# Kernel optimization log

Hardware: AMD Instinct MI355X
Metric: run time of the kernel (lower is better)

Reference implementation:

```python
import jax, jax.numpy as jnp
import numpy as np

N = 50000      # number of nodes
E = 800000     # number of edges (avg degree 16)
DIN = 128
DOUT = 128
EPS = 1e-06


def setup_inputs() -> dict:
    key = jax.random.key(0)
    ks = jax.random.split(key, 10)
    scale = 1.0 / np.sqrt(DIN)
    return {
        "mean": jax.random.normal(ks[0], (N, DIN), dtype=jnp.float32),
        "var": jax.random.uniform(ks[1], (N, DIN), dtype=jnp.float32),
        "W_mean": jax.random.normal(ks[2], (DIN, DOUT), dtype=jnp.float32) * scale,
        "b_mean": jax.random.normal(ks[3], (DOUT,), dtype=jnp.float32) * scale,
        "W_var": jax.random.normal(ks[4], (DIN, DOUT), dtype=jnp.float32) * scale,
        "b_var": jax.random.normal(ks[5], (DOUT,), dtype=jnp.float32) * scale,
        "adj0_w": jax.random.uniform(ks[6], (E,), dtype=jnp.float32),
        "adj1_w": jax.random.uniform(ks[7], (E,), dtype=jnp.float32),
        "edge_src": jax.random.randint(ks[8], (E,), 0, N, dtype=jnp.int32),
        "edge_dst": jax.random.randint(ks[9], (E,), 0, N, dtype=jnp.int32),
    }


def reference(mean, var, W_mean, b_mean, W_var, b_var, adj0_w, adj1_w, edge_src, edge_dst):
    # Dense projections (dropout is identity in eval mode)
    m = jax.nn.elu(mean @ W_mean + b_mean)            # [N, DOUT]
    v = jax.nn.relu(var @ W_var + b_var) + EPS        # [N, DOUT]
    # Elementwise attention gate
    att = jnp.exp(-v)
    m = m * att
    v = v * att * att
    # SpMM aggregation: out[dst] += w * x[src]  (COO edge list)
    n = mean.shape[0]
    out_m = jax.ops.segment_sum(adj0_w[:, None] * m[edge_src], edge_dst, num_segments=n)
    out_v = jax.ops.segment_sum(adj1_w[:, None] * v[edge_src], edge_dst, num_segments=n)
    return out_m, out_v
```

## Files before the change

kernel.cpp:

```cpp
#include <hip/hip_runtime.h>
#include <hip/hip_bf16.h>
#include <math.h>

#define N_NODES 50000
#define DIN     128
#define DOUT    128
#define EPS_    1e-6f
#define N_WAVES 3125
#define NBKT    196
#define EPB     4096
#define SLOT_CAP 5120

typedef __attribute__((ext_vector_type(8))) short  bf16x8;
typedef __attribute__((ext_vector_type(4))) float  f32x4;
typedef unsigned short ushort_t;

__device__ __forceinline__ ushort_t f2bf(float f) {
    unsigned u = __float_as_uint(f);
    return (ushort_t)((u + 0x7fffu + ((u >> 16) & 1u)) >> 16);
}
__device__ __forceinline__ float bflo(unsigned u) { return __uint_as_float(u << 16); }
__device__ __forceinline__ float bfhi(unsigned u) { return __uint_as_float(u & 0xffff0000u); }

__global__ __launch_bounds__(256) void prep_w_kernel(
    const float* __restrict__ Wm, const float* __restrict__ Wv,
    ushort_t* __restrict__ fm, ushort_t* __restrict__ fv,
    int* __restrict__ gcur)
{
    const int gid = blockIdx.x * 256 + threadIdx.x;
    if (gid < NBKT) gcur[gid] = 0;
    const int k = gid >> 7, n = gid & 127;
    const int ct = n >> 4, kk = k >> 5, quad = (k >> 3) & 3, j = k & 7;
    const int idx = ((ct * 4 + kk) * 64 + quad * 16 + (n & 15)) * 8 + j;
    fm[idx] = f2bf(Wm[gid]);
    fv[idx] = f2bf(Wv[gid]);
}

__global__ __launch_bounds__(256) void proj_mfma_kernel(
    const float* __restrict__ mean, const float* __restrict__ var,
    const float* __restrict__ bm,   const float* __restrict__ bv,
    const ushort_t* __restrict__ wfm, const ushort_t* __restrict__ wfv,
    ushort_t* __restrict__ mv)
{
    const int wave = blockIdx.x * 4 + (threadIdx.x >> 6);
    if (wave >= N_WAVES) return;
    const int lane = threadIdx.x & 63;
    const int row0 = wave * 16;
    const int kq   = lane >> 4;
    const int arow = row0 + (lane & 15);

    f32x4 accm[8], accv[8];
#pragma unroll
    for (int ct = 0; ct < 8; ++ct) {
        accm[ct] = (f32x4){0.f, 0.f, 0.f, 0.f};
        accv[ct] = (f32x4){0.f, 0.f, 0.f, 0.f};
    }

    const float* mrow = mean + (size_t)arow * DIN;
    const float* vrow = var  + (size_t)arow * DIN;

#pragma unroll
    for (int kk = 0; kk < 4; ++kk) {
        const int kb = kk * 32 + kq * 8;
        const float4 am0 = *(const float4*)(mrow + kb);
        const float4 am1 = *(const float4*)(mrow + kb + 4);
        const float4 av0 = *(const float4*)(vrow + kb);
        const float4 av1 = *(const float4*)(vrow + kb + 4);
        bf16x8 a_m, a_v;
        a_m[0]=f2bf(am0.x); a_m[1]=f2bf(am0.y); a_m[2]=f2bf(am0.z); a_m[3]=f2bf(am0.w);
        a_m[4]=f2bf(am1.x); a_m[5]=f2bf(am1.y); a_m[6]=f2bf(am1.z); a_m[7]=f2bf(am1.w);
        a_v[0]=f2bf(av0.x); a_v[1]=f2bf(av0.y); a_v[2]=f2bf(av0.z); a_v[3]=f2bf(av0.w);
        a_v[4]=f2bf(av1.x); a_v[5]=f2bf(av1.y); a_v[6]=f2bf(av1.z); a_v[7]=f2bf(av1.w);

#pragma unroll
        for (int ct = 0; ct < 8; ++ct) {
            const bf16x8 b_m = *(const bf16x8*)(wfm + ((size_t)(ct * 4 + kk) * 64 + lane) * 8);
            const bf16x8 b_v = *(const bf16x8*)(wfv + ((size_t)(ct * 4 + kk) * 64 + lane) * 8);
            accm[ct] = __builtin_amdgcn_mfma_f32_16x16x32_bf16(a_m, b_m, accm[ct], 0, 0, 0);
            accv[ct] = __builtin_amdgcn_mfma_f32_16x16x32_bf16(a_v, b_v, accv[ct], 0, 0, 0);
        }
    }

#pragma unroll
    for (int ct = 0; ct < 8; ++ct) {
        const int col = ct * 16 + (lane & 15);
        const float bmc = bm[col];
        const float bvc = bv[col];
        const int pbase = (col >> 1) * 4 + (col & 1);
#pragma unroll
        for (int r = 0; r < 4; ++r) {
            const int row = row0 + kq * 4 + r;
            float m = accm[ct][r] + bmc;
            m = (m > 0.0f) ? m : (expf(m) - 1.0f);
            float v = accv[ct][r] + bvc;
            v = ((v > 0.0f) ? v : 0.0f) + EPS_;
            const float att = expf(-v);
            ushort_t* rowp = mv + (size_t)row * 256;
            rowp[pbase]     = f2bf(m * att);
            rowp[pbase + 2] = f2bf(v * att * att);
        }
    }
}

__global__ __launch_bounds__(256) void bucketA_kernel(
    const int* __restrict__ src, const int* __restrict__ dst,
    const float* __restrict__ w0, const float* __restrict__ w1,
    int* __restrict__ gcur, uint2* __restrict__ slots, int E)
{
    __shared__ uint2 s_rec[EPB];
    __shared__ int   s_gpos[EPB];
    __shared__ int   s_hist[256];
    __shared__ int   s_scn[256];
    __shared__ int   s_cur[256];
    __shared__ int   s_base[256];

    const int t  = threadIdx.x;
    const int e0 = blockIdx.x * EPB;
    const int n  = min(EPB, E - e0);

    s_hist[t] = 0;
    __syncthreads();

    int   myb[16];
    uint2 myr[16];
#pragma unroll
    for (int j = 0; j < 16; ++j) {
        const int e = e0 + t + j * 256;
        if (e < E) {
            const int d = dst[e];
            const int b = d >> 8;
            myb[j] = b;
            myr[j].x = (unsigned)src[e] | ((unsigned)(d & 255) << 16);
            myr[j].y = (unsigned)f2bf(w0[e]) | ((unsigned)f2bf(w1[e]) << 16);
            atomicAdd(&s_hist[b], 1);
        } else myb[j] = -1;
    }
    __syncthreads();

    if (t < NBKT) {
        const int c = s_hist[t];
        s_base[t] = t * SLOT_CAP + (c ? atomicAdd(&gcur[t], c) : 0);
    }
    const int x = s_hist[t];
    s_scn[t] = x;
    __syncthreads();
    for (int off = 1; off < 256; off <<= 1) {
        const int v = (t >= off) ? s_scn[t - off] : 0;
        __syncthreads();
        s_scn[t] += v;
        __syncthreads();
    }
    const int excl = s_scn[t] - x;
    __syncthreads();
    s_scn[t] = excl;
    s_cur[t] = 0;
    __syncthreads();

#pragma unroll
    for (int j = 0; j < 16; ++j) {
        if (myb[j] >= 0) {
            const int r = atomicAdd(&s_cur[myb[j]], 1);
            const int p = s_scn[myb[j]] + r;
            s_rec[p]  = myr[j];
            s_gpos[p] = s_base[myb[j]] + r;
        }
    }
    __syncthreads();

    for (int i = t; i < n; i += 256)
        slots[s_gpos[i]] = s_rec[i];
}

__global__ __launch_bounds__(256) void bucketB_kernel(
    const int* __restrict__ gcur,
    const uint2* __restrict__ slots, uint2* __restrict__ final_e,
    int* __restrict__ node_start)
{
    __shared__ int s_hist[256];
    __shared__ int s_scn[256];
    __shared__ int s_cur[256];
    __shared__ int s_red[256];

    const int b = blockIdx.x;
    const int t = threadIdx.x;

    s_red[t] = (t < b) ? gcur[t] : 0;
    s_hist[t] = 0;
    __syncthreads();
    for (int off = 128; off > 0; off >>= 1) {
        if (t < off) s_red[t] += s_red[t + off];
        __syncthreads();
    }
    const int base = s_red[0];
    const int cnt  = gcur[b];
    const uint2* slot = slots + (size_t)b * SLOT_CAP;

    uint2 myr[20];
    int   myf[20];
    int   k = 0;
    for (int i = t; i < cnt; i += 256) {
        const uint2 r = slot[i];
        const int f = (r.x >> 16) & 255;
        myr[k] = r; myf[k] = f; ++k;
        atomicAdd(&s_hist[f], 1);
    }
    __syncthreads();

    const int x = s_hist[t];
    s_scn[t] = x;
    __syncthreads();
    for (int off = 1; off < 256; off <<= 1) {
        const int v = (t >= off) ? s_scn[t - off] : 0;
        __syncthreads();
        s_scn[t] += v;
        __syncthreads();
    }
    const int excl = s_scn[t] - x;
    __syncthreads();

    const int gidx = b * 256 + t;
    if (gidx <= N_NODES) node_start[gidx] = base + excl;

    s_cur[t] = excl;
    __syncthreads();

#pragma unroll
    for (int j = 0; j < 20; ++j) {
        if (j < k) {
            const int p = atomicAdd(&s_cur[myf[j]], 1);
            final_e[base + p] = myr[j];
        }
    }
}

#define PAIR_FMA(RW, G) do {                                                 \
    const float a0 = bflo(RW), a1 = bfhi(RW);                                \
    am0 = fmaf(a0, bflo((G).x), am0); am1 = fmaf(a0, bfhi((G).x), am1);      \
    av0 = fmaf(a1, bflo((G).y), av0); av1 = fmaf(a1, bfhi((G).y), av1);      \
    am2 = fmaf(a0, bflo((G).z), am2); am3 = fmaf(a0, bfhi((G).z), am3);      \
    av2 = fmaf(a1, bflo((G).w), av2); av3 = fmaf(a1, bfhi((G).w), av3);      \
} while (0)

__global__ __launch_bounds__(256) void agg_kernel(
    const ushort_t* __restrict__ mv,
    const uint2* __restrict__ edges, const int* __restrict__ node_start,
    float* __restrict__ out_m, float* __restrict__ out_v)
{
    const int node = blockIdx.x * 4 + (threadIdx.x >> 6);
    const int lane = threadIdx.x & 63;
    const int half = lane >> 5;
    const int l    = lane & 31;
    if (node >= N_NODES) return;

    const int j0 = node_start[node];
    const int j1 = node_start[node + 1];

    float am0=0.f, am1=0.f, am2=0.f, am3=0.f;
    float av0=0.f, av1=0.f, av2=0.f, av3=0.f;

    int j = j0;

    if ((j & 1) && j < j1) {
        const uint2 r = edges[j];
        const unsigned rw = half ? 0u : r.y;
        const uint4 g = *(const uint4*)(mv + (size_t)(r.x & 0xffffu) * 256 + l * 8);
        PAIR_FMA(rw, g);
        ++j;
    }

    for (; j + 8 <= j1; j += 8) {
        const uint4 e0 = *(const uint4*)(edges + j + 0);
        const uint4 e1 = *(const uint4*)(edges + j + 2);
        const uint4 e2 = *(const uint4*)(edges + j + 4);
        const uint4 e3 = *(const uint4*)(edges + j + 6);
        const unsigned s0 = half ? e0.z : e0.x, w0 = half ? e0.w : e0.y;
        const unsigned s1 = half ? e1.z : e1.x, w1 = half ? e1.w : e1.y;
        const unsigned s2 = half ? e2.z : e2.x, w2 = half ? e2.w : e2.y;
        const unsigned s3 = half ? e3.z : e3.x, w3 = half ? e3.w : e3.y;
        const uint4 g0 = *(const uint4*)(mv + (size_t)(s0 & 0xffffu) * 256 + l * 8);
        const uint4 g1 = *(const uint4*)(mv + (size_t)(s1 & 0xffffu) * 256 + l * 8);
        const uint4 g2 = *(const uint4*)(mv + (size_t)(s2 & 0xffffu) * 256 + l * 8);
        const uint4 g3 = *(const uint4*)(mv + (size_t)(s3 & 0xffffu) * 256 + l * 8);
        PAIR_FMA(w0, g0);
        PAIR_FMA(w1, g1);
        PAIR_FMA(w2, g2);
        PAIR_FMA(w3, g3);
    }

    for (; j + 2 <= j1; j += 2) {
        const uint4 e = *(const uint4*)(edges + j);
        const unsigned s = half ? e.z : e.x, w = half ? e.w : e.y;
        const uint4 g = *(const uint4*)(mv + (size_t)(s & 0xffffu) * 256 + l * 8);
        PAIR_FMA(w, g);
    }

    if (j < j1) {
        const uint2 r = edges[j];
        const unsigned rw = half ? 0u : r.y;
        const uint4 g = *(const uint4*)(mv + (size_t)(r.x & 0xffffu) * 256 + l * 8);
        PAIR_FMA(rw, g);
    }

    am0 += __shfl_xor(am0, 32); am1 += __shfl_xor(am1, 32);
    am2 += __shfl_xor(am2, 32); am3 += __shfl_xor(am3, 32);
    av0 += __shfl_xor(av0, 32); av1 += __shfl_xor(av1, 32);
    av2 += __shfl_xor(av2, 32); av3 += __shfl_xor(av3, 32);

    if (half == 0) {
        *(float4*)(out_m + (size_t)node * DOUT + l * 4) = make_float4(am0, am1, am2, am3);
        *(float4*)(out_v + (size_t)node * DOUT + l * 4) = make_float4(av0, av1, av2, av3);
    }
}

extern "C" void kernel_launch(void* const* d_in, const int* in_sizes, int n_in,
                              void* d_out, int out_size, void* d_ws, size_t ws_size,
                              hipStream_t stream) {
    const float* mean = (const float*)d_in[0];
    const float* var  = (const float*)d_in[1];
    const float* Wm   = (const float*)d_in[2];
    const float* bm   = (const float*)d_in[3];
    const float* Wv   = (const float*)d_in[4];
    const float* bv   = (const float*)d_in[5];
    const float* a0   = (const float*)d_in[6];
    const float* a1   = (const float*)d_in[7];
    const int*   es   = (const int*)d_in[8];
    const int*   ed   = (const int*)d_in[9];
    const int    E    = in_sizes[6];

    char* ws = (char*)d_ws;
    ushort_t* mv        = (ushort_t*)ws;
    uint2* slots        = (uint2*)(ws + 25600000);
    uint2* final_e      = (uint2*)(ws + 33628160);
    int*   node_start   = (int*)  (ws + 40028160);
    int*   gcur         = (int*)  (ws + 40228176);
    ushort_t* wfm       = (ushort_t*)(ws + 40228976);
    ushort_t* wfv       = wfm + 16384;

    float* out_m = (float*)d_out;
    float* out_v = out_m + (size_t)N_NODES * DOUT;

    prep_w_kernel<<<64, 256, 0, stream>>>(Wm, Wv, wfm, wfv, gcur);

    proj_mfma_kernel<<<(N_WAVES + 3) / 4, 256, 0, stream>>>(
        mean, var, bm, bv, wfm, wfv, mv);

    bucketA_kernel<<<(E + EPB - 1) / EPB, 256, 0, stream>>>(
        es, ed, a0, a1, gcur, slots, E);
    bucketB_kernel<<<NBKT, 256, 0, stream>>>(
        gcur, slots, final_e, node_start);

    agg_kernel<<<(N_NODES + 3) / 4, 256, 0, stream>>>(
        mv, final_e, node_start, out_m, out_v);
}
```

Baseline: 232.7 us.

## Fuse projection and edge bucketing into one launch; stream bucketB from global

Merges the MFMA projection kernel and the first edge-bucketing pass into a single launch, with the first nA blocks doing bucketing and the rest doing projection. The two independent phases can then overlap on the GPU and one launch is saved. The cost is that the projection blocks now carry the bucketing kernel's large shared-memory allocation, which may lower occupancy. bucketB also stops caching records in registers and re-reads each slot from global memory in a second pass, cutting register use at the price of an extra read.

```diff
diff --git a/kernel.cpp b/kernel.cpp
--- a/kernel.cpp
+++ b/kernel.cpp
@@ -10,6 +10,7 @@
 #define NBKT    196
 #define EPB     4096
 #define SLOT_CAP 5120
+#define NB_PROJ 782
 
 typedef __attribute__((ext_vector_type(8))) short  bf16x8;
 typedef __attribute__((ext_vector_type(4))) float  f32x4;
@@ -36,13 +37,82 @@
     fv[idx] = f2bf(Wv[gid]);
 }
 
-__global__ __launch_bounds__(256) void proj_mfma_kernel(
+__global__ __launch_bounds__(256) void fused_projA_kernel(
     const float* __restrict__ mean, const float* __restrict__ var,
     const float* __restrict__ bm,   const float* __restrict__ bv,
     const ushort_t* __restrict__ wfm, const ushort_t* __restrict__ wfv,
-    ushort_t* __restrict__ mv)
+    ushort_t* __restrict__ mv,
+    const int* __restrict__ src, const int* __restrict__ dst,
+    const float* __restrict__ w0, const float* __restrict__ w1,
+    int* __restrict__ gcur, uint2* __restrict__ slots, int E, int nA)
 {
-    const int wave = blockIdx.x * 4 + (threadIdx.x >> 6);
+    if ((int)blockIdx.x < nA) {
+        __shared__ uint2 s_rec[EPB];
+        __shared__ int   s_gpos[EPB];
+        __shared__ int   s_hist[256];
+        __shared__ int   s_scn[256];
+        __shared__ int   s_cur[256];
+        __shared__ int   s_base[256];
+
+        const int t  = threadIdx.x;
+        const int e0 = blockIdx.x * EPB;
+        const int n  = min(EPB, E - e0);
+
+        s_hist[t] = 0;
+        __syncthreads();
+
+        int   myb[16];
+        uint2 myr[16];
+#pragma unroll
+        for (int j = 0; j < 16; ++j) {
+            const int e = e0 + t + j * 256;
+            if (e < E) {
+                const int d = dst[e];
+                const int b = d >> 8;
+                myb[j] = b;
+                myr[j].x = (unsigned)src[e] | ((unsigned)(d & 255) << 16);
+                myr[j].y = (unsigned)f2bf(w0[e]) | ((unsigned)f2bf(w1[e]) << 16);
+                atomicAdd(&s_hist[b], 1);
+            } else myb[j] = -1;
+        }
+        __syncthreads();
+
+        if (t < NBKT) {
+            const int c = s_hist[t];
+            s_base[t] = t * SLOT_CAP + (c ? atomicAdd(&gcur[t], c) : 0);
+        }
+        const int x = s_hist[t];
+        s_scn[t] = x;
+        __syncthreads();
+        for (int off = 1; off < 256; off <<= 1) {
+            const int v = (t >= off) ? s_scn[t - off] : 0;
+            __syncthreads();
+            s_scn[t] += v;
+            __syncthreads();
+        }
+        const int excl = s_scn[t] - x;
+        __syncthreads();
+        s_scn[t] = excl;
+        s_cur[t] = 0;
+        __syncthreads();
+
+#pragma unroll
+        for (int j = 0; j < 16; ++j) {
+            if (myb[j] >= 0) {
+                const int r = atomicAdd(&s_cur[myb[j]], 1);
+                const int p = s_scn[myb[j]] + r;
+                s_rec[p]  = myr[j];
+                s_gpos[p] = s_base[myb[j]] + r;
+            }
+        }
+        __syncthreads();
+
+        for (int i = t; i < n; i += 256)
+            slots[s_gpos[i]] = s_rec[i];
+        return;
+    }
+
+    const int wave = ((int)blockIdx.x - nA) * 4 + (threadIdx.x >> 6);
     if (wave >= N_WAVES) return;
     const int lane = threadIdx.x & 63;
     const int row0 = wave * 16;
@@ -102,75 +172,6 @@
     }
 }
 
-__global__ __launch_bounds__(256) void bucketA_kernel(
-    const int* __restrict__ src, const int* __restrict__ dst,
-    const float* __restrict__ w0, const float* __restrict__ w1,
-    int* __restrict__ gcur, uint2* __restrict__ slots, int E)
-{
-    __shared__ uint2 s_rec[EPB];
-    __shared__ int   s_gpos[EPB];
-    __shared__ int   s_hist[256];
-    __shared__ int   s_scn[256];
-    __shared__ int   s_cur[256];
-    __shared__ int   s_base[256];
-
-    const int t  = threadIdx.x;
-    const int e0 = blockIdx.x * EPB;
-    const int n  = min(EPB, E - e0);
-
-    s_hist[t] = 0;
-    __syncthreads();
-
-    int   myb[16];
-    uint2 myr[16];
-#pragma unroll
-    for (int j = 0; j < 16; ++j) {
-        const int e = e0 + t + j * 256;
-        if (e < E) {
-            const int d = dst[e];
-            const int b = d >> 8;
-            myb[j] = b;
-            myr[j].x = (unsigned)src[e] | ((unsigned)(d & 255) << 16);
-            myr[j].y = (unsigned)f2bf(w0[e]) | ((unsigned)f2bf(w1[e]) << 16);
-            atomicAdd(&s_hist[b], 1);
-        } else myb[j] = -1;
-    }
-    __syncthreads();
-
-    if (t < NBKT) {
-        const int c = s_hist[t];
-        s_base[t] = t * SLOT_CAP + (c ? atomicAdd(&gcur[t], c) : 0);
-    }
-    const int x = s_hist[t];
-    s_scn[t] = x;
-    __syncthreads();
-    for (int off = 1; off < 256; off <<= 1) {
-        const int v = (t >= off) ? s_scn[t - off] : 0;
-        __syncthreads();
-        s_scn[t] += v;
-        __syncthreads();
-    }
-    const int excl = s_scn[t] - x;
-    __syncthreads();
-    s_scn[t] = excl;
-    s_cur[t] = 0;
-    __syncthreads();
-
-#pragma unroll
-    for (int j = 0; j < 16; ++j) {
-        if (myb[j] >= 0) {
-            const int r = atomicAdd(&s_cur[myb[j]], 1);
-            const int p = s_scn[myb[j]] + r;
-            s_rec[p]  = myr[j];
-            s_gpos[p] = s_base[myb[j]] + r;
-        }
-    }
-    __syncthreads();
-
-    for (int i = t; i < n; i += 256)
-        slots[s_gpos[i]] = s_rec[i];
-}
-
 __global__ __launch_bounds__(256) void bucketB_kernel(
     const int* __restrict__ gcur,
     const uint2* __restrict__ slots, uint2* __restrict__ final_e,
@@ -184,7 +185,7 @@
     const int b = blockIdx.x;
     const int t = threadIdx.x;
 
-    s_red[t] = (t < b) ? gcur[t] : 0;
+    s_red[t]  = (t < b) ? gcur[t] : 0;
     s_hist[t] = 0;
     __syncthreads();
     for (int off = 128; off > 0; off >>= 1) {
@@ -195,41 +196,33 @@
     const int cnt  = gcur[b];
     const uint2* slot = slots + (size_t)b * SLOT_CAP;
 
-    uint2 myr[20];
-    int   myf[20];
-    int   k = 0;
+    for (int i = t; i < cnt; i += 256)
+        atomicAdd(&s_hist[(slot[i].x >> 16) & 255], 1);
+    __syncthreads();
+
+    const int x = s_hist[t];
+    s_scn[t] = x;
+    __syncthreads();
+    for (int off = 1; off < 256; off <<= 1) {
+        const int v = (t >= off) ? s_scn[t - off] : 0;
+        __syncthreads();
+        s_scn[t] += v;
+        __syncthreads();
+    }
+    const int excl = s_scn[t] - x;
+    __syncthreads();
+
+    const int gidx = b * 256 + t;
+    if (gidx <= N_NODES) node_start[gidx] = base + excl;
+
+    s_cur[t] = excl;
+    __syncthreads();
+
     for (int i = t; i < cnt; i += 256) {
         const uint2 r = slot[i];
         const int f = (r.x >> 16) & 255;
-        myr[k] = r; myf[k] = f; ++k;
-        atomicAdd(&s_hist[f], 1);
-    }
-    __syncthreads();
-
-    const int x = s_hist[t];
-    s_scn[t] = x;
-    __syncthreads();
-    for (int off = 1; off < 256; off <<= 1) {
-        const int v = (t >= off) ? s_scn[t - off] : 0;
-        __syncthreads();
-        s_scn[t] += v;
-        __syncthreads();
-    }
-    const int excl = s_scn[t] - x;
-    __syncthreads();
-
-    const int gidx = b * 256 + t;
-    if (gidx <= N_NODES) node_start[gidx] = base + excl;
-
-    s_cur[t] = excl;
-    __syncthreads();
-
-#pragma unroll
-    for (int j = 0; j < 20; ++j) {
-        if (j < k) {
-            const int p = atomicAdd(&s_cur[myf[j]], 1);
-            final_e[base + p] = myr[j];
-        }
+        const int p = atomicAdd(&s_cur[f], 1);
+        final_e[base + p] = r;
     }
 }
 
@@ -341,11 +334,11 @@
 
     prep_w_kernel<<<64, 256, 0, stream>>>(Wm, Wv, wfm, wfv, gcur);
 
-    proj_mfma_kernel<<<(N_WAVES + 3) / 4, 256, 0, stream>>>(
-        mean, var, bm, bv, wfm, wfv, mv);
-
-    bucketA_kernel<<<(E + EPB - 1) / EPB, 256, 0, stream>>>(
-        es, ed, a0, a1, gcur, slots, E);
+    const int nA = (E + EPB - 1) / EPB;
+    fused_projA_kernel<<<nA + NB_PROJ, 256, 0, stream>>>(
+        mean, var, bm, bv, wfm, wfv, mv,
+        es, ed, a0, a1, gcur, slots, E, nA);
+
     bucketB_kernel<<<NBKT, 256, 0, stream>>>(
         gcur, slots, final_e, node_start);
 
```

Result: faster. 211.8 us (-9.0%).
